# Kernel tuning notes

Measured on AMD Instinct MI355X. Metric: run time of the kernel, lower is better.

The kernel has to match this reference:

```python
import jax, jax.numpy as jnp
from jax import lax
import numpy as np

GRID_SIZE = 3
SPLINE_ORDER = 2
N_BASIS = GRID_SIZE + SPLINE_ORDER  # 5
_H = 2.0 / GRID_SIZE  # grid_range [-1, 1]
# extended uniform grid, shape (1, grid_size + 2*spline_order + 1) = (1, 8)
GRID = (jnp.arange(-SPLINE_ORDER, GRID_SIZE + SPLINE_ORDER + 1, dtype=jnp.float32) * _H - 1.0)[None, :]


def b_splines(x):
    """Cox-de Boor B-spline bases. x: (..., F) -> (..., F, N_BASIS)."""
    x = x[..., None]
    g = GRID
    bases = ((x >= g[:, :-1]) & (x < g[:, 1:])).astype(x.dtype)
    for p in range(1, SPLINE_ORDER + 1):
        left = (x - g[:, :-(p + 1)]) / (g[:, p:-1] - g[:, :-(p + 1)])
        right = (g[:, p + 1:] - x) / (g[:, p + 1:] - g[:, 1:-p])
        bases = left * bases[..., :-1] + right * bases[..., 1:]
    return bases


def kan_conv(x, base_w, spline_w, scaler):
    """Unfold-based KAN conv: x NCHW -> NCHW. base_w (O,F), spline_w (O,F,K), scaler (O,F)."""
    # patches: (B, C*kh*kw, H', W'), channel-major feature ordering like torch unfold
    p = lax.conv_general_dilated_patches(x, (4, 4), (2, 2), ((1, 1), (1, 1)))
    f = jnp.transpose(p, (0, 2, 3, 1))  # (B, H', W', F)
    base = jax.nn.relu(f) @ base_w.T
    spl = jnp.einsum('bhwfk,ofk->bhwo', b_splines(f), spline_w * scaler[..., None])
    return jnp.transpose(base + spl, (0, 3, 1, 2))


def batchnorm(x, gamma, beta):
    # train-mode BN over (B,H,W) per channel, eps=1e-5 (torch default)
    m = x.mean((0, 2, 3), keepdims=True)
    v = x.var((0, 2, 3), keepdims=True)
    return (x - m) * lax.rsqrt(v + 1e-5) * gamma[None, :, None, None] + beta[None, :, None, None]


def setup_inputs() -> dict:
    key = jax.random.key(0)
    ks = jax.random.split(key, 32)
    B = 512
    chans = [(3, 32), (32, 64), (64, 128), (128, 128)]
    inp = {"x": jax.random.normal(ks[0], (B, 3, 32, 32), jnp.float32)}
    i = 1
    for li, (cin, cout) in enumerate(chans, start=1):
        F = cin * 16
        inp[f"bw{li}"] = jax.random.normal(ks[i], (cout, F), jnp.float32) * (0.8 / np.sqrt(F)); i += 1
        inp[f"sw{li}"] = jax.random.normal(ks[i], (cout, F, N_BASIS), jnp.float32) * (0.8 / np.sqrt(F)); i += 1
        inp[f"sc{li}"] = jnp.ones((cout, F), jnp.float32) + 0.05 * jax.random.normal(ks[i], (cout, F), jnp.float32); i += 1
    for bi, c in [(1, 64), (2, 128), (3, 128)]:
        inp[f"g{bi}"] = jnp.ones((c,), jnp.float32)
        inp[f"b{bi}"] = jnp.zeros((c,), jnp.float32)
    inp["fc_w"] = jax.random.normal(ks[i], (1, 128), jnp.float32) * (1.0 / np.sqrt(128)); i += 1
    inp["fc_b"] = jnp.zeros((1,), jnp.float32)
    return inp


def reference(x, bw1, sw1, sc1, bw2, sw2, sc2, bw3, sw3, sc3, bw4, sw4, sc4,
              g1, b1, g2, b2, g3, b3, fc_w, fc_b):
    h = kan_conv(x, bw1, sw1, sc1)                     # (B,32,16,16)
    h = kan_conv(h, bw2, sw2, sc2)                     # (B,64,8,8)
    h = batchnorm(h, g1, b1)
    h = kan_conv(h, bw3, sw3, sc3)                     # (B,128,4,4)
    h = batchnorm(h, g2, b2)
    h = kan_conv(h, bw4, sw4, sc4)                     # (B,128,2,2)
    h = batchnorm(h, g3, b3)
    h = h.mean((2, 3))                                 # AdaptiveAvgPool2d(1) + Flatten -> (B,128)
    return jax.nn.sigmoid(h @ fc_w.T + fc_b)           # (B,1)
```

## Files before the change

### kernel.cpp

```cpp
#include <hip/hip_runtime.h>
#include <hip/hip_bf16.h>
#include <math.h>

#define DEVINL __device__ __forceinline__

typedef short short8 __attribute__((ext_vector_type(8)));
typedef float f32x4 __attribute__((ext_vector_type(4)));

DEVINL unsigned short f2bf(float f) {
    union { float f; unsigned int u; } c; c.f = f;
    unsigned int u = c.u;
    return (unsigned short)((u + 0x7fffu + ((u >> 16) & 1u)) >> 16);
}

DEVINL unsigned int packbf2(float a, float b) {
    union { __hip_bfloat162 h; unsigned int u; } c;
    c.h = __float22bfloat162_rn(make_float2(a, b));
    return c.u;
}

DEVINL void gload_lds16(const unsigned int* g, unsigned int* l) {
    __builtin_amdgcn_global_load_lds((const __attribute__((address_space(1))) unsigned int*)g,
                                     (__attribute__((address_space(3))) unsigned int*)l, 16, 0, 0);
}

DEVINL uint4 expand_frag(float v) {
    float relu = fmaxf(v, 0.f);
    float u = fmaf(v, 1.5f, 3.5f);
    float fj = floorf(u);
    int j = (int)fj;
    float t = u - fj;
    float omt = 1.f - t;
    float v2 = 0.5f * omt * omt;
    float v1 = fmaf(t, omt, 0.5f);
    float v0 = 0.5f * t * t;
    float b[5];
#pragma unroll
    for (int i = 0; i < 5; ++i)
        b[i] = (i == j) ? v0 : (i == j - 1) ? v1 : (i == j - 2) ? v2 : 0.f;
    uint4 r;
    r.x = packbf2(relu, b[0]);
    r.y = packbf2(b[1], b[2]);
    r.z = packbf2(b[3], b[4]);
    r.w = 0u;
    return r;
}

DEVINL void prep_one(int idx, int F, int NTT, const float* __restrict__ bw,
                     const float* __restrict__ sw, const float* __restrict__ sc,
                     unsigned short* __restrict__ wf) {
    int j = idx & 7;
    int lane = (idx >> 3) & 63;
    int t = idx >> 9;
    int ks = t & 3;
    int t2 = t >> 2;
    int nt = t2 % NTT;
    int c = t2 / NTT;
    int k = ks * 32 + ((lane >> 4) << 3) + j;
    int tap = k >> 3, s = k & 7;
    int f = c * 16 + tap;
    int o = nt * 16 + (lane & 15);
    float v = 0.f;
    if (s == 0) v = bw[o * F + f];
    else if (s <= 5) v = sw[(o * F + f) * 5 + (s - 1)] * sc[o * F + f];
    wf[idx] = f2bf(v);
}

__global__ __launch_bounds__(256) void prep_all(
    const float* __restrict__ bw1, const float* __restrict__ sw1, const float* __restrict__ sc1,
    const float* __restrict__ bw2, const float* __restrict__ sw2, const float* __restrict__ sc2,
    const float* __restrict__ bw3, const float* __restrict__ sw3, const float* __restrict__ sc3,
    const float* __restrict__ bw4, const float* __restrict__ sw4, const float* __restrict__ sc4,
    unsigned short* __restrict__ wf1, unsigned short* __restrict__ wf2,
    unsigned short* __restrict__ wf3, unsigned short* __restrict__ wf4) {
    int idx = blockIdx.x * 256 + threadIdx.x;
    const int N1 = 3 * 32 * 128;
    const int N2 = 32 * 64 * 128;
    const int N3 = 64 * 128 * 128;
    const int N4 = 128 * 128 * 128;
    if (idx < N1) prep_one(idx, 48, 2, bw1, sw1, sc1, wf1);
    else if (idx < N1 + N2) prep_one(idx - N1, 512, 4, bw2, sw2, sc2, wf2);
    else if (idx < N1 + N2 + N3) prep_one(idx - N1 - N2, 1024, 8, bw3, sw3, sc3, wf3);
    else if (idx < N1 + N2 + N3 + N4) prep_one(idx - N1 - N2 - N3, 2048, 8, bw4, sw4, sc4, wf4);
}

template <int CIN, int COUT, int HOUT, int WOUT, int WM, int WN, int MT, int CPS,
          int UB, bool HASBN, int BNS, int NBN, bool SPLITOUT, int RPAD>
__global__ __launch_bounds__(256) void kan_conv_fused(
    const float* __restrict__ in, const unsigned short* __restrict__ wf,
    const float* __restrict__ part, const float* __restrict__ gamma,
    const float* __restrict__ beta, float* __restrict__ out) {
    constexpr int HIN = HOUT * 2, WIN = WOUT * 2, W2 = WOUT;
    constexpr int NT = COUT / 16;
    constexpr int NTW = NT / WN;
    constexpr int BM = WM * MT * 16;
    constexpr int IMG_POS = HOUT * WOUT;
    constexpr int NIMG = BM / IMG_POS;
    constexpr int RS = WIN + RPAD;
    constexpr int IMG_STRIDE = HIN * RS + 1;
    constexpr int ASLOTS = NIMG * IMG_STRIDE + 1;
    constexpr int M_TOT = 512 * IMG_POS;
    constexpr int EV = NIMG * HIN * WIN;
    constexpr int EITER = (EV + 255) / 256;
    static_assert(WM * WN == 4, "4 waves");
    static_assert(CPS % UB == 0, "UB divides CPS");

    __shared__ uint4 A_e[UB][ASLOTS];
    __shared__ uint4 B_l[UB][COUT * 16];

    const int tid = threadIdx.x;
    const int lane = tid & 63;
    const int w = tid >> 6;
    const int wm = w % WM;
    const int wn = w / WM;
    const int g = lane >> 4;
    const int r16 = lane & 15;
    const int m0 = blockIdx.x * BM;
    const int b0 = m0 / IMG_POS;
    const int c0 = SPLITOUT ? blockIdx.y * CPS : 0;

    int aoff[MT];
    int vmask = 0;
#pragma unroll
    for (int mt = 0; mt < MT; ++mt) {
        int p = (wm * MT + mt) * 16 + r16;
        int m = m0 + p;
        int ow = m % WOUT;
        int oh = (m / WOUT) % HOUT;
        int bl = p / IMG_POS;
        int iw = 2 * ow - 1 + g;
        bool iv = (iw >= 0) && (iw < WIN);
        aoff[mt] = 1 + bl * IMG_STRIDE + (2 * oh) * RS + (iw & 1) * W2 + (iw >> 1);
#pragma unroll
        for (int ks = 0; ks < 4; ++ks) {
            bool vv = iv && !(oh == 0 && ks == 0) && !(oh == HOUT - 1 && ks == 3);
            vmask |= (vv ? 1 : 0) << (mt * 4 + ks);
        }
    }

    if (tid < UB) A_e[tid][0] = expand_frag(0.f);

    f32x4 acc[MT][NTW];
#pragma unroll
    for (int mt = 0; mt < MT; ++mt)
#pragma unroll
        for (int n = 0; n < NTW; ++n) acc[mt][n] = f32x4{0.f, 0.f, 0.f, 0.f};

    for (int cc = 0; cc < CPS; cc += UB) {
#pragma unroll
        for (int u = 0; u < UB; ++u) {
            const int ch = c0 + cc + u;
            const unsigned int* bsrc = (const unsigned int*)(wf + (size_t)ch * (COUT * 128));
            unsigned int* bdst = (unsigned int*)&B_l[u][0];
#pragma unroll
            for (int r2 = 0; r2 < NT; ++r2)
                gload_lds16(bsrc + ((r2 << 8) + tid) * 4, bdst + ((r2 << 8) + tid) * 4);
        }
#pragma unroll
        for (int u = 0; u < UB; ++u) {
            const int ch = c0 + cc + u;
            float bsc = 1.f, bsh = 0.f;
            if (HASBN) {
                float sm = 0.f, s2 = 0.f;
#pragma unroll 4
                for (int s = 0; s < BNS; ++s) {
                    sm += part[(ch * BNS + s) * 2];
                    s2 += part[(ch * BNS + s) * 2 + 1];
                }
                const float invN = 1.f / (float)NBN;
                float mean = sm * invN;
                float var = s2 * invN - mean * mean;
                float rs = rsqrtf(var + 1e-5f);
                bsc = gamma[ch] * rs;
                bsh = beta[ch] - mean * bsc;
            }
#pragma unroll
            for (int ii = 0; ii < EITER; ++ii) {
                int e = tid + ii * 256;
                if ((EV % 256 == 0) || e < EV) {
                    int bl = e / (HIN * WIN);
                    int r = e - bl * (HIN * WIN);
                    int ih = r / WIN;
                    int iw = r - ih * WIN;
                    float v = in[(((size_t)(b0 + bl) * CIN + ch) * HIN + ih) * WIN + iw];
                    if (HASBN) v = fmaf(v, bsc, bsh);
                    A_e[u][1 + bl * IMG_STRIDE + ih * RS + (iw & 1) * W2 + (iw >> 1)] = expand_frag(v);
                }
            }
        }
        __syncthreads();
#pragma unroll
        for (int u = 0; u < UB; ++u) {
#pragma unroll
            for (int ks = 0; ks < 4; ++ks) {
                short8 bf[NTW];
#pragma unroll
                for (int n = 0; n < NTW; ++n)
                    bf[n] = *(const short8*)&B_l[u][(((wn * NTW + n) * 4 + ks) << 6) + lane];
#pragma unroll
                for (int mt = 0; mt < MT; ++mt) {
                    int slot = ((vmask >> (mt * 4 + ks)) & 1) ? (aoff[mt] + (ks - 1) * RS) : 0;
                    short8 af = *(const short8*)&A_e[u][slot];
#pragma unroll
                    for (int n = 0; n < NTW; ++n)
                        acc[mt][n] = __builtin_amdgcn_mfma_f32_16x16x32_bf16(af, bf[n], acc[mt][n], 0, 0, 0);
                }
            }
        }
        __syncthreads();
    }

    const int colo = lane & 15;
    const int row4 = (lane >> 4) * 4;
#pragma unroll
    for (int mt = 0; mt < MT; ++mt) {
#pragma unroll
        for (int n = 0; n < NTW; ++n) {
            int o = (wn * NTW + n) * 16 + colo;
#pragma unroll
            for (int rr = 0; rr < 4; ++rr) {
                int p = (wm * MT + mt) * 16 + row4 + rr;
                int m = m0 + p;
                if (SPLITOUT) {
                    out[((size_t)blockIdx.y * M_TOT + m) * COUT + o] = acc[mt][n][rr];
                } else {
                    int ow = m % WOUT;
                    int t = m / WOUT;
                    int oh = t % HOUT;
                    int b = t / HOUT;
                    out[((b * COUT + o) * HOUT + oh) * WOUT + ow] = acc[mt][n][rr];
                }
            }
        }
    }
}

template <int NS, int COUT, int HOUT, int WOUT>
__global__ __launch_bounds__(256) void reduce_split(const float* __restrict__ P,
                                                    float* __restrict__ out) {
    constexpr int M = 512 * HOUT * WOUT;
    int idx4 = blockIdx.x * 256 + threadIdx.x;
    if (idx4 >= M * COUT / 4) return;
    f32x4 s = {0.f, 0.f, 0.f, 0.f};
#pragma unroll
    for (int i = 0; i < NS; ++i) {
        f32x4 v = *(const f32x4*)&P[(size_t)i * M * COUT + idx4 * 4];
        s += v;
    }
    int o0 = (idx4 * 4) % COUT;
    int m = (idx4 * 4) / COUT;
    int ow = m % WOUT;
    int t = m / WOUT;
    int oh = t % HOUT;
    int b = t / HOUT;
#pragma unroll
    for (int q = 0; q < 4; ++q)
        out[((b * COUT + o0 + q) * HOUT + oh) * WOUT + ow] = s[q];
}

template <int C, int HW, int S>
__global__ __launch_bounds__(256) void bn_partial(const float* __restrict__ a,
                                                  float* __restrict__ part) {
    constexpr int BS = 512 / S;
    constexpr int NE = BS * HW;
    int c = blockIdx.x / S, s = blockIdx.x % S;
    int tid = threadIdx.x;
    float sm = 0.f, s2 = 0.f;
    for (int e = tid; e < NE; e += 256) {
        int b = s * BS + e / HW;
        int hw = e % HW;
        float v = a[((size_t)b * C + c) * HW + hw];
        sm += v;
        s2 += v * v;
    }
    __shared__ float r0[256], r1[256];
    r0[tid] = sm; r1[tid] = s2;
    __syncthreads();
    for (int off = 128; off > 0; off >>= 1) {
        if (tid < off) { r0[tid] += r0[tid + off]; r1[tid] += r1[tid + off]; }
        __syncthreads();
    }
    if (tid == 0) {
        part[(c * S + s) * 2] = r0[0];
        part[(c * S + s) * 2 + 1] = r1[0];
    }
}

__global__ void head_ker(const float* __restrict__ a4, const float* __restrict__ part3,
                         const float* __restrict__ g3, const float* __restrict__ b3,
                         const float* __restrict__ fcw, const float* __restrict__ fcb,
                         float* __restrict__ out) {
    int b = blockIdx.x;
    int lane = threadIdx.x;
    float acc = 0.0f;
#pragma unroll
    for (int j = 0; j < 2; ++j) {
        int o = lane + 64 * j;
        float sm = 0.f, s2 = 0.f;
#pragma unroll
        for (int s = 0; s < 8; ++s) {
            sm += part3[(o * 8 + s) * 2];
            s2 += part3[(o * 8 + s) * 2 + 1];
        }
        float mean = sm * (1.f / 2048.f);
        float var = s2 * (1.f / 2048.f) - mean * mean;
        float rs = rsqrtf(var + 1e-5f);
        float scl = g3[o] * rs;
        float sh = b3[o] - mean * scl;
        const float* p = a4 + (b * 128 + o) * 4;
        float sv = p[0] + p[1] + p[2] + p[3];
        float pooled = fmaf(sv * 0.25f, scl, sh);
        acc = fmaf(pooled, fcw[o], acc);
    }
#pragma unroll
    for (int off = 32; off > 0; off >>= 1) acc += __shfl_down(acc, off);
    if (lane == 0) out[b] = 1.0f / (1.0f + expf(-(acc + fcb[0])));
}

extern "C" void kernel_launch(void* const* d_in, const int* in_sizes, int n_in,
                              void* d_out, int out_size, void* d_ws, size_t ws_size,
                              hipStream_t stream) {
    const float* x   = (const float*)d_in[0];
    const float* bw1 = (const float*)d_in[1];
    const float* sw1 = (const float*)d_in[2];
    const float* sc1 = (const float*)d_in[3];
    const float* bw2 = (const float*)d_in[4];
    const float* sw2 = (const float*)d_in[5];
    const float* sc2 = (const float*)d_in[6];
    const float* bw3 = (const float*)d_in[7];
    const float* sw3 = (const float*)d_in[8];
    const float* sc3 = (const float*)d_in[9];
    const float* bw4 = (const float*)d_in[10];
    const float* sw4 = (const float*)d_in[11];
    const float* sc4 = (const float*)d_in[12];
    const float* g1  = (const float*)d_in[13];
    const float* b1  = (const float*)d_in[14];
    const float* g2  = (const float*)d_in[15];
    const float* b2  = (const float*)d_in[16];
    const float* g3  = (const float*)d_in[17];
    const float* b3  = (const float*)d_in[18];
    const float* fcw = (const float*)d_in[19];
    const float* fcb = (const float*)d_in[20];

    float* ws = (float*)d_ws;
    float* a1 = ws;
    float* a2 = a1 + 4194304;
    float* a3 = a2 + 2097152;
    float* a4 = a3 + 1048576;
    unsigned short* wf1 = (unsigned short*)(a4 + 262144);
    unsigned short* wf2 = wf1 + 12288;
    unsigned short* wf3 = wf2 + 262144;
    unsigned short* wf4 = wf3 + 1048576;
    float* part1 = (float*)(wf4 + 2097152);
    float* part2 = part1 + 2048;
    float* part3 = part2 + 4096;
    float* P3 = a1;
    float* P4 = a2;

    prep_all<<<13360, 256, 0, stream>>>(bw1, sw1, sc1, bw2, sw2, sc2,
                                        bw3, sw3, sc3, bw4, sw4, sc4,
                                        wf1, wf2, wf3, wf4);

    kan_conv_fused<3, 32, 16, 16, 4, 1, 4, 3, 3, false, 1, 1, false, 0>
        <<<512, 256, 0, stream>>>(x, wf1, nullptr, nullptr, nullptr, a1);
    kan_conv_fused<32, 64, 8, 8, 2, 2, 2, 32, 2, false, 1, 1, false, 0>
        <<<512, 256, 0, stream>>>(a1, wf2, nullptr, nullptr, nullptr, a2);
    bn_partial<64, 64, 16><<<1024, 256, 0, stream>>>(a2, part1);
    kan_conv_fused<64, 128, 4, 4, 1, 4, 4, 16, 2, true, 16, 32768, true, 1>
        <<<dim3(128, 4), 256, 0, stream>>>(a2, wf3, part1, g1, b1, P3);
    reduce_split<4, 128, 4, 4><<<1024, 256, 0, stream>>>(P3, a3);
    bn_partial<128, 16, 16><<<2048, 256, 0, stream>>>(a3, part2);
    kan_conv_fused<128, 128, 2, 2, 1, 4, 2, 16, 2, true, 16, 8192, true, 0>
        <<<dim3(64, 8), 256, 0, stream>>>(a3, wf4, part2, g2, b2, P4);
    reduce_split<8, 128, 2, 2><<<256, 256, 0, stream>>>(P4, a4);
    bn_partial<128, 4, 8><<<1024, 256, 0, stream>>>(a4, part3);
    head_ker<<<512, 64, 0, stream>>>(a4, part3, g3, b3, fcw, fcb, (float*)d_out);
}
```

Measured before the change: 146.5 us.

## Split output channels across grid blocks in KAN conv layers 2-4

```diff
diff --git a/kernel.cpp b/kernel.cpp
--- a/kernel.cpp
+++ b/kernel.cpp
@@ -84,13 +84,15 @@
     else if (idx < N1 + N2 + N3 + N4) prep_one(idx - N1 - N2 - N3, 2048, 8, bw4, sw4, sc4, wf4);
 }
 
-template <int CIN, int COUT, int HOUT, int WOUT, int WM, int WN, int MT, int CPS,
-          int UB, bool HASBN, int BNS, int NBN, bool SPLITOUT, int RPAD>
+template <int CIN, int COUTT, int NSP, int HOUT, int WOUT, int WM, int WN, int MT,
+          int CPS, int UB, bool HASBN, int BNS, int NBN, bool SPLITOUT, int RPAD>
 __global__ __launch_bounds__(256) void kan_conv_fused(
     const float* __restrict__ in, const unsigned short* __restrict__ wf,
     const float* __restrict__ part, const float* __restrict__ gamma,
     const float* __restrict__ beta, float* __restrict__ out) {
     constexpr int HIN = HOUT * 2, WIN = WOUT * 2, W2 = WOUT;
+    constexpr int COUT = COUTT / NSP;
+    constexpr int NTT = COUTT / 16;
     constexpr int NT = COUT / 16;
     constexpr int NTW = NT / WN;
     constexpr int BM = WM * MT * 16;
@@ -117,7 +119,9 @@
     const int r16 = lane & 15;
     const int m0 = blockIdx.x * BM;
     const int b0 = m0 / IMG_POS;
-    const int c0 = SPLITOUT ? blockIdx.y * CPS : 0;
+    const int nh = (NSP > 1) ? ((int)blockIdx.y % NSP) : 0;
+    const int kslice = (NSP > 1) ? ((int)blockIdx.y / NSP) : (SPLITOUT ? (int)blockIdx.y : 0);
+    const int c0 = SPLITOUT ? kslice * CPS : 0;
 
     int aoff[MT];
     int vmask = 0;
@@ -150,11 +154,11 @@
 #pragma unroll
         for (int u = 0; u < UB; ++u) {
             const int ch = c0 + cc + u;
-            const unsigned int* bsrc = (const unsigned int*)(wf + (size_t)ch * (COUT * 128));
+            const unsigned int* bsrc = (const unsigned int*)wf + ((size_t)ch * NTT + nh * NT) * 1024;
             unsigned int* bdst = (unsigned int*)&B_l[u][0];
 #pragma unroll
             for (int r2 = 0; r2 < NT; ++r2)
-                gload_lds16(bsrc + ((r2 << 8) + tid) * 4, bdst + ((r2 << 8) + tid) * 4);
+                gload_lds16(bsrc + (r2 << 10) + tid * 4, bdst + (r2 << 10) + tid * 4);
         }
 #pragma unroll
         for (int u = 0; u < UB; ++u) {
@@ -216,19 +220,19 @@
     for (int mt = 0; mt < MT; ++mt) {
 #pragma unroll
         for (int n = 0; n < NTW; ++n) {
-            int o = (wn * NTW + n) * 16 + colo;
+            int o = nh * COUT + (wn * NTW + n) * 16 + colo;
 #pragma unroll
             for (int rr = 0; rr < 4; ++rr) {
                 int p = (wm * MT + mt) * 16 + row4 + rr;
                 int m = m0 + p;
                 if (SPLITOUT) {
-                    out[((size_t)blockIdx.y * M_TOT + m) * COUT + o] = acc[mt][n][rr];
+                    out[((size_t)kslice * M_TOT + m) * COUTT + o] = acc[mt][n][rr];
                 } else {
                     int ow = m % WOUT;
                     int t = m / WOUT;
                     int oh = t % HOUT;
                     int b = t / HOUT;
-                    out[((b * COUT + o) * HOUT + oh) * WOUT + ow] = acc[mt][n][rr];
+                    out[((b * COUTT + o) * HOUT + oh) * WOUT + ow] = acc[mt][n][rr];
                 }
             }
         }
@@ -361,17 +365,17 @@
                                         bw3, sw3, sc3, bw4, sw4, sc4,
                                         wf1, wf2, wf3, wf4);
 
-    kan_conv_fused<3, 32, 16, 16, 4, 1, 4, 3, 3, false, 1, 1, false, 0>
+    kan_conv_fused<3, 32, 1, 16, 16, 4, 1, 4, 3, 3, false, 1, 1, false, 0>
         <<<512, 256, 0, stream>>>(x, wf1, nullptr, nullptr, nullptr, a1);
-    kan_conv_fused<32, 64, 8, 8, 2, 2, 2, 32, 2, false, 1, 1, false, 0>
-        <<<512, 256, 0, stream>>>(a1, wf2, nullptr, nullptr, nullptr, a2);
+    kan_conv_fused<32, 64, 2, 8, 8, 4, 1, 2, 32, 4, false, 1, 1, false, 0>
+        <<<dim3(256, 2), 256, 0, stream>>>(a1, wf2, nullptr, nullptr, nullptr, a2);
     bn_partial<64, 64, 16><<<1024, 256, 0, stream>>>(a2, part1);
-    kan_conv_fused<64, 128, 4, 4, 1, 4, 4, 16, 2, true, 16, 32768, true, 1>
-        <<<dim3(128, 4), 256, 0, stream>>>(a2, wf3, part1, g1, b1, P3);
+    kan_conv_fused<64, 128, 2, 4, 4, 4, 1, 2, 16, 2, true, 16, 32768, true, 1>
+        <<<dim3(64, 8), 256, 0, stream>>>(a2, wf3, part1, g1, b1, P3);
     reduce_split<4, 128, 4, 4><<<1024, 256, 0, stream>>>(P3, a3);
     bn_partial<128, 16, 16><<<2048, 256, 0, stream>>>(a3, part2);
-    kan_conv_fused<128, 128, 2, 2, 1, 4, 2, 16, 2, true, 16, 8192, true, 0>
-        <<<dim3(64, 8), 256, 0, stream>>>(a3, wf4, part2, g2, b2, P4);
+    kan_conv_fused<128, 128, 2, 2, 2, 4, 1, 1, 16, 2, true, 16, 8192, true, 0>
+        <<<dim3(32, 16), 256, 0, stream>>>(a3, wf4, part2, g2, b2, P4);
     reduce_split<8, 128, 2, 2><<<256, 256, 0, stream>>>(P4, a4);
     bn_partial<128, 4, 8><<<1024, 256, 0, stream>>>(a4, part3);
     head_ker<<<512, 64, 0, stream>>>(a4, part3, g3, b3, fcw, fcb, (float*)d_out);
```

New measurement: 144.7 us. About the same (-1.3%).
